# Performance work log

Measured on AMD Instinct MI355X. Metric: run time of the kernel, lower is better.

Reference implementation:

```python
import jax, jax.numpy as jnp
import numpy as np

EPS = 1e-12  # torch F.normalize default eps

def _l2norm(x):
    # torch.nn.functional.normalize(x, dim=-1): x / max(||x||_2, eps)
    n = jnp.linalg.norm(x, axis=-1, keepdims=True)
    return x / jnp.maximum(n, EPS)

def setup_inputs() -> dict:
    key = jax.random.key(0)
    ks = jax.random.split(key, 12)
    B, T, D, V, C = 16, 2048, 1024, 32000, 6
    s = 0.02
    text = jax.random.randint(ks[0], (B * T,), 0, V, dtype=jnp.int64)
    offsets = (jnp.arange(B, dtype=jnp.int64) * T)  # uniform-length sequences
    emb = jax.random.normal(ks[1], (V, D), dtype=jnp.float32) * s
    Wq = jax.random.normal(ks[2], (D, D), dtype=jnp.float32) * s
    bq = jnp.zeros((D,), jnp.float32)
    Wk = jax.random.normal(ks[3], (D, D), dtype=jnp.float32) * s
    bk = jnp.zeros((D,), jnp.float32)
    Wv = jax.random.normal(ks[4], (D, D), dtype=jnp.float32) * s
    bv = jnp.zeros((D,), jnp.float32)
    Wfc = jax.random.normal(ks[5], (D, D), dtype=jnp.float32) * s
    bfc = jnp.zeros((D,), jnp.float32)
    Wo = jax.random.normal(ks[6], (C, D), dtype=jnp.float32) * s
    bo = jnp.zeros((C,), jnp.float32)
    return {"text": text, "offsets": offsets, "emb": emb,
            "Wq": Wq, "bq": bq, "Wk": Wk, "bk": bk, "Wv": Wv, "bv": bv,
            "Wfc": Wfc, "bfc": bfc, "Wo": Wo, "bo": bo}

def reference(text, offsets, emb, Wq, bq, Wk, bk, Wv, bv, Wfc, bfc, Wo, bo):
    B = offsets.shape[0]
    T = text.shape[0] // B  # uniform lengths -> pad_sequence == reshape
    D = emb.shape[1]
    tok = text.reshape(B, T)
    x = emb[tok]                                   # [B,T,D]
    q = x @ Wq.T + bq
    k = x @ Wk.T + bk
    v = x @ Wv.T + bv
    scores = jnp.einsum('bqd,bkd->bqk', q, k) / jnp.sqrt(jnp.asarray(D, x.dtype))
    causal = jnp.tril(jnp.ones((T, T), dtype=bool))
    scores = jnp.where(causal[None, :, :], scores, -jnp.inf)
    attn = jax.nn.softmax(scores, axis=-1)
    out = jnp.einsum('bqk,bkd->bqd', attn, v) + x  # residual with embedding
    out = _l2norm(out)
    out = out + (out @ Wfc.T + bfc)                # residual FFN
    out = _l2norm(out)
    last = out[:, -1, :]                           # [B,D]
    return jax.nn.sigmoid(last @ Wo.T + bo)        # [B,num_class]
```

## Files before the change

kernel.cpp:

```cpp
#include <hip/hip_runtime.h>
#include <hip/hip_bf16.h>
#include <math.h>

typedef unsigned short ushort_t;

__device__ __forceinline__ float bf2f(ushort_t u) {
    union { unsigned int i; float f; } v;
    v.i = ((unsigned int)u) << 16;
    return v.f;
}

__device__ __forceinline__ ushort_t f2bf(float f) {
    union { float f; unsigned int i; } v; v.f = f;
    unsigned int lsb = (v.i >> 16) & 1;
    unsigned int r = v.i + 0x7FFF + lsb;
    return (ushort_t)(r >> 16);
}

__device__ __forceinline__ float wave_sum(float acc) {
    #pragma unroll
    for (int off = 32; off >= 1; off >>= 1) acc += __shfl_xor(acc, off, 64);
    return acc;
}
__device__ __forceinline__ float wave_max(float acc) {
    #pragma unroll
    for (int off = 32; off >= 1; off >>= 1) acc = fmaxf(acc, __shfl_xor(acc, off, 64));
    return acc;
}

__device__ __forceinline__ void ld8(const void* p, int isbf, size_t i, float* o) {
    if (isbf) {
        uint4 raw = *reinterpret_cast<const uint4*>((const ushort_t*)p + i);
        const ushort_t* pu = reinterpret_cast<const ushort_t*>(&raw);
        #pragma unroll
        for (int k = 0; k < 8; ++k) o[k] = bf2f(pu[k]);
    } else {
        const float4* f = reinterpret_cast<const float4*>((const float*)p + i);
        float4 a = f[0], b = f[1];
        o[0]=a.x; o[1]=a.y; o[2]=a.z; o[3]=a.w;
        o[4]=b.x; o[5]=b.y; o[6]=b.z; o[7]=b.w;
    }
}

__device__ __forceinline__ void ld4(const void* p, int isbf, size_t i, float* o) {
    if (isbf) {
        uint2 raw = *reinterpret_cast<const uint2*>((const ushort_t*)p + i);
        const ushort_t* pu = reinterpret_cast<const ushort_t*>(&raw);
        #pragma unroll
        for (int k = 0; k < 4; ++k) o[k] = bf2f(pu[k]);
    } else {
        float4 a = *reinterpret_cast<const float4*>((const float*)p + i);
        o[0]=a.x; o[1]=a.y; o[2]=a.z; o[3]=a.w;
    }
}

__device__ __forceinline__ float ldS(const void* p, int isbf, size_t i) {
    return isbf ? bf2f(((const ushort_t*)p)[i]) : ((const float*)p)[i];
}

__device__ __forceinline__ int tokAt(const void* text, int isi64, size_t i) {
    return isi64 ? ((const int*)text)[2 * i] : ((const int*)text)[i];
}

__device__ __forceinline__ void detect_flags(const void* emb, const void* text, int* sf) {
    if (threadIdx.x < 64) {
        const int lane = threadIdx.x;
        ushort_t u = ((const ushort_t*)emb)[2 * lane];
        int e = (u >> 7) & 0xFF;
        unsigned long long mb = __ballot(e >= 0x60 && e <= 0x7E);
        int odd = ((const int*)text)[2 * lane + 1];
        unsigned long long mi = __ballot(odd != 0);
        if (lane == 0) {
            sf[0] = (__popcll(mb) >= 32) ? 1 : 0;
            sf[1] = (__popcll(mi) == 0) ? 1 : 0;
        }
    }
    __syncthreads();
}

__device__ __forceinline__ void hoist16(const float* v, int lane, float* c16) {
    #pragma unroll
    for (int k = 0; k < 16; ++k) c16[k] = v[lane * 16 + k];
}

__global__ void kQC(const void* __restrict__ text, const void* __restrict__ emb,
                    const void* __restrict__ Wq, const void* __restrict__ bq,
                    const void* __restrict__ Wk, float* __restrict__ c_part,
                    int B, int T, int D) {
    const int nch = D >> 6;
    const int b = blockIdx.x / nch;
    const int ch = blockIdx.x % nch;
    const int i0 = ch << 6;
    const int tid = threadIdx.x;
    __shared__ int sf[2];
    __shared__ float xs[1024];
    __shared__ float qs[64];
    detect_flags(emb, text, sf);
    const int isbf = sf[0], isi64 = sf[1];
    const int tok = tokAt(text, isi64, (size_t)b * T + (T - 1));
    float w4[4];
    for (int dd = tid * 4; dd < D; dd += 1024) {
        ld4(emb, isbf, (size_t)tok * D + dd, w4);
        xs[dd]=w4[0]; xs[dd+1]=w4[1]; xs[dd+2]=w4[2]; xs[dd+3]=w4[3];
    }
    __syncthreads();
    const int wave = tid >> 6, lane = tid & 63;
    float c16[16];
    hoist16(xs, lane, c16);
    float w[8];
    for (int r = 0; r < 16; ++r) {
        const int i = i0 + wave * 16 + r;
        float acc = 0.f;
        ld8(Wq, isbf, (size_t)i * D + lane * 16, w);
        #pragma unroll
        for (int k = 0; k < 8; ++k) acc += w[k] * c16[k];
        ld8(Wq, isbf, (size_t)i * D + lane * 16 + 8, w);
        #pragma unroll
        for (int k = 0; k < 8; ++k) acc += w[k] * c16[8 + k];
        acc = wave_sum(acc);
        if (lane == 0) qs[wave * 16 + r] = acc + ldS(bq, isbf, i);
    }
    __syncthreads();
    const int d = tid * 4;
    float a0=0.f, a1=0.f, a2=0.f, a3=0.f;
    #pragma unroll 8
    for (int i = 0; i < 64; ++i) {
        const float qv = qs[i];
        ld4(Wk, isbf, (size_t)(i0 + i) * D + d, w4);
        a0 += qv*w4[0]; a1 += qv*w4[1]; a2 += qv*w4[2]; a3 += qv*w4[3];
    }
    *reinterpret_cast<float4*>(c_part + ((size_t)ch * B + b) * D + d)
        = make_float4(a0, a1, a2, a3);
}

__global__ void k35(const void* __restrict__ text, const void* __restrict__ emb,
                    const float* __restrict__ c_part, float* __restrict__ xbar_part,
                    float* __restrict__ m_part, float* __restrict__ l_part,
                    int B, int T, int D, int nch_c, float scale) {
    const int nch = T >> 5;
    const int b = blockIdx.x / nch;
    const int ch = blockIdx.x % nch;
    const int j0 = ch << 5;
    const int tid = threadIdx.x;
    __shared__ int sf[2];
    __shared__ ushort_t rows[32 * 1024];
    __shared__ float cs[1024];
    __shared__ float sjs[32];
    __shared__ float wls[32];
    __shared__ int tks[32];
    detect_flags(emb, text, sf);
    const int isbf = sf[0], isi64 = sf[1];
    {
        const int d = tid * 4;
        float4 acc = make_float4(0.f, 0.f, 0.f, 0.f);
        for (int cc = 0; cc < nch_c; ++cc) {
            float4 v = *reinterpret_cast<const float4*>(c_part + ((size_t)cc * B + b) * D + d);
            acc.x += v.x; acc.y += v.y; acc.z += v.z; acc.w += v.w;
        }
        cs[d]=acc.x; cs[d+1]=acc.y; cs[d+2]=acc.z; cs[d+3]=acc.w;
    }
    if (tid < 32) tks[tid] = tokAt(text, isi64, (size_t)b * T + j0 + tid);
    __syncthreads();
    if (isbf) {
        const ushort_t* E = (const ushort_t*)emb;
        const int half = tid >> 7;
        const int off  = (tid & 127) * 8;
        #pragma unroll 4
        for (int sw = 0; sw < 16; ++sw) {
            const int r = sw * 2 + half;
            uint4 v = *reinterpret_cast<const uint4*>(E + (size_t)tks[r] * D + off);
            *reinterpret_cast<uint4*>(&rows[r * 1024 + off]) = v;
        }
    }
    __syncthreads();
    const int wave = tid >> 6, lane = tid & 63;
    {
        float c16[16];
        hoist16(cs, lane, c16);
        float w[8];
        for (int rr = 0; rr < 8; ++rr) {
            const int r = wave + rr * 4;
            float acc = 0.f;
            if (isbf) {
                uint4 raw = *reinterpret_cast<const uint4*>(&rows[r * 1024 + lane * 16]);
                const ushort_t* pu = reinterpret_cast<const ushort_t*>(&raw);
                #pragma unroll
                for (int k = 0; k < 8; ++k) acc += bf2f(pu[k]) * c16[k];
                raw = *reinterpret_cast<const uint4*>(&rows[r * 1024 + lane * 16 + 8]);
                #pragma unroll
                for (int k = 0; k < 8; ++k) acc += bf2f(pu[k]) * c16[8 + k];
            } else {
                ld8(emb, 0, (size_t)tks[r] * D + lane * 16, w);
                #pragma unroll
                for (int k = 0; k < 8; ++k) acc += w[k] * c16[k];
                ld8(emb, 0, (size_t)tks[r] * D + lane * 16 + 8, w);
                #pragma unroll
                for (int k = 0; k < 8; ++k) acc += w[k] * c16[8 + k];
            }
            acc = wave_sum(acc);
            if (lane == 0) sjs[r] = acc * scale;
        }
    }
    __syncthreads();
    float mx = -INFINITY;
    #pragma unroll
    for (int j = 0; j < 32; ++j) mx = fmaxf(mx, sjs[j]);
    if (tid < 32) wls[tid] = expf(sjs[tid] - mx);
    __syncthreads();
    if (tid < 64) {
        float v = (tid < 32) ? wls[tid] : 0.f;
        v = wave_sum(v);
        if (tid == 0) { m_part[ch * B + b] = mx; l_part[ch * B + b] = v; }
    }
    const int d = tid * 4;
    float a0=0.f, a1=0.f, a2=0.f, a3=0.f;
    if (isbf) {
        #pragma unroll 8
        for (int j = 0; j < 32; ++j) {
            const float wj = wls[j];
            uint2 raw = *reinterpret_cast<const uint2*>(&rows[j * 1024 + d]);
            const ushort_t* pu = reinterpret_cast<const ushort_t*>(&raw);
            a0 += wj*bf2f(pu[0]); a1 += wj*bf2f(pu[1]);
            a2 += wj*bf2f(pu[2]); a3 += wj*bf2f(pu[3]);
        }
    } else {
        float w4[4];
        #pragma unroll 8
        for (int j = 0; j < 32; ++j) {
            const float wj = wls[j];
            ld4(emb, 0, (size_t)tks[j] * D + d, w4);
            a0 += wj*w4[0]; a1 += wj*w4[1]; a2 += wj*w4[2]; a3 += wj*w4[3];
        }
    }
    *reinterpret_cast<float4*>(xbar_part + ((size_t)ch * B + b) * D + d)
        = make_float4(a0, a1, a2, a3);
}

__global__ void kCA(const void* __restrict__ text, const void* __restrict__ emb,
                    const float* __restrict__ xbar_part, const float* __restrict__ m_part,
                    const float* __restrict__ l_part, const void* __restrict__ Wv,
                    const void* __restrict__ bv, float* __restrict__ u,
                    int B, int T, int D, int nch_k) {
    const int nb = D >> 5;
    const int b = blockIdx.x / nb;
    const int r0 = (blockIdx.x % nb) << 5;
    const int tid = threadIdx.x;
    __shared__ int sf[2];
    __shared__ float xb[1024];
    __shared__ float sc[64];
    __shared__ float xl32[32];
    detect_flags(emb, text, sf);
    const int isbf = sf[0], isi64 = sf[1];
    const int tok = tokAt(text, isi64, (size_t)b * T + (T - 1));
    if (tid < 32) xl32[tid] = ldS(emb, isbf, (size_t)tok * D + r0 + tid);
    if (tid < 64) {
        float mv = (tid < nch_k) ? m_part[tid * B + b] : -INFINITY;
        float mx = wave_max(mv);
        float e  = (tid < nch_k) ? expf(mv - mx) : 0.f;
        float lv = (tid < nch_k) ? l_part[tid * B + b] * e : 0.f;
        float lg = wave_sum(lv);
        sc[tid] = e / lg;
    }
    __syncthreads();
    {
        const int d = tid * 4;
        float4 acc = make_float4(0.f, 0.f, 0.f, 0.f);
        for (int cc = 0; cc < nch_k; ++cc) {
            const float s = sc[cc];
            float4 v = *reinterpret_cast<const float4*>(xbar_part + ((size_t)cc * B + b) * D + d);
            acc.x += s*v.x; acc.y += s*v.y; acc.z += s*v.z; acc.w += s*v.w;
        }
        xb[d]=acc.x; xb[d+1]=acc.y; xb[d+2]=acc.z; xb[d+3]=acc.w;
    }
    __syncthreads();
    const int wave = tid >> 6, lane = tid & 63;
    float c16[16];
    hoist16(xb, lane, c16);
    float w[8];
    for (int rr = 0; rr < 8; ++rr) {
        const int i = r0 + wave + rr * 4;
        float acc = 0.f;
        ld8(Wv, isbf, (size_t)i * D + lane * 16, w);
        #pragma unroll
        for (int k = 0; k < 8; ++k) acc += w[k] * c16[k];
        ld8(Wv, isbf, (size_t)i * D + lane * 16 + 8, w);
        #pragma unroll
        for (int k = 0; k < 8; ++k) acc += w[k] * c16[8 + k];
        acc = wave_sum(acc);
        if (lane == 0) u[b * D + i] = acc + ldS(bv, isbf, i) + xl32[i - r0];
    }
}

__global__ void k6c_h2(const void* __restrict__ text, const void* __restrict__ emb,
                       const void* __restrict__ Wfc, const void* __restrict__ bfc,
                       const float* __restrict__ u, float* __restrict__ h2, int D) {
    const int nb = D >> 5;
    const int b = blockIdx.x / nb;
    const int r0 = (blockIdx.x % nb) << 5;
    const int tid = threadIdx.x;
    __shared__ int sf[2];
    __shared__ float hs[1024];
    __shared__ float red[256];
    __shared__ float s_rn;
    detect_flags(emb, text, sf);
    const int isbf = sf[0];
    float part = 0.f;
    {
        const int dd = tid * 4;
        float4 v = *reinterpret_cast<const float4*>(u + b * D + dd);
        hs[dd]=v.x; hs[dd+1]=v.y; hs[dd+2]=v.z; hs[dd+3]=v.w;
        part = v.x*v.x + v.y*v.y + v.z*v.z + v.w*v.w;
    }
    red[tid] = part;
    __syncthreads();
    for (int st = 128; st; st >>= 1) {
        if (tid < st) red[tid] += red[tid + st];
        __syncthreads();
    }
    if (tid == 0) s_rn = 1.f / fmaxf(sqrtf(red[0]), 1e-12f);
    __syncthreads();
    const float rn = s_rn;
    {
        const int dd = tid * 4;
        hs[dd] *= rn; hs[dd+1] *= rn; hs[dd+2] *= rn; hs[dd+3] *= rn;
    }
    __syncthreads();
    const int wave = tid >> 6, lane = tid & 63;
    float c16[16];
    hoist16(hs, lane, c16);
    float w[8];
    for (int rr = 0; rr < 8; ++rr) {
        const int i = r0 + wave + rr * 4;
        float acc = 0.f;
        ld8(Wfc, isbf, (size_t)i * D + lane * 16, w);
        #pragma unroll
        for (int k = 0; k < 8; ++k) acc += w[k] * c16[k];
        ld8(Wfc, isbf, (size_t)i * D + lane * 16 + 8, w);
        #pragma unroll
        for (int k = 0; k < 8; ++k) acc += w[k] * c16[8 + k];
        acc = wave_sum(acc);
        if (lane == 0) h2[b * D + i] = hs[i] + acc + ldS(bfc, isbf, i);
    }
}

__global__ void k6d_out(const void* __restrict__ text, const void* __restrict__ emb,
                        const void* __restrict__ Wo, const void* __restrict__ bo,
                        const float* __restrict__ h2, void* __restrict__ out,
                        int D, int C, int total) {
    __shared__ int sf[2];
    detect_flags(emb, text, sf);
    const int isbf = sf[0];
    const int g = blockIdx.x * 4 + (threadIdx.x >> 6);
    if (g >= total) return;
    const int lane = threadIdx.x & 63;
    const int b = g / C, ci = g % C;
    float a1 = 0.f, a2 = 0.f, w[8], h[8];
    for (int d0 = lane * 8; d0 < D; d0 += 512) {
        ld8(Wo, isbf, (size_t)ci * D + d0, w);
        ld8(h2, 0, (size_t)b * D + d0, h);
        #pragma unroll
        for (int k = 0; k < 8; ++k) { a1 += w[k] * h[k]; a2 += h[k] * h[k]; }
    }
    a1 = wave_sum(a1);
    a2 = wave_sum(a2);
    if (lane == 0) {
        float rn = 1.f / fmaxf(sqrtf(a2), 1e-12f);
        float z = a1 * rn + ldS(bo, isbf, ci);
        float y = 1.f / (1.f + expf(-z));
        if (isbf) ((ushort_t*)out)[g] = f2bf(y);
        else      ((float*)out)[g] = y;
    }
}

extern "C" void kernel_launch(void* const* d_in, const int* in_sizes, int n_in,
                              void* d_out, int out_size, void* d_ws, size_t ws_size,
                              hipStream_t stream) {
    const void* text = d_in[0];
    const void* emb = d_in[2];
    const void* Wq  = d_in[3];
    const void* bq  = d_in[4];
    const void* Wk  = d_in[5];
    const void* Wv  = d_in[7];
    const void* bv  = d_in[8];
    const void* Wfc = d_in[9];
    const void* bfc = d_in[10];
    const void* Wo  = d_in[11];
    const void* bo  = d_in[12];

    const int B = in_sizes[1];
    const int T = in_sizes[0] / B;
    const int D = in_sizes[4];
    const int C = in_sizes[12];

    const int nch_c = D / 64;
    const int nch_k = T / 32;

    float* ws        = (float*)d_ws;
    float* c_part    = ws;
    float* xbar_part = c_part + (size_t)nch_c * B * D;
    float* m_part    = xbar_part + (size_t)nch_k * B * D;
    float* l_part    = m_part + (size_t)nch_k * B;
    float* u         = l_part + (size_t)nch_k * B;
    float* h2        = u + (size_t)B * D;

    const float scale = 1.0f / sqrtf((float)D);

    kQC<<<B * (D / 64), 256, 0, stream>>>(text, emb, Wq, bq, Wk, c_part, B, T, D);
    k35<<<B * (T / 32), 256, 0, stream>>>(text, emb, c_part, xbar_part, m_part, l_part,
                                          B, T, D, nch_c, scale);
    kCA<<<B * (D / 32), 256, 0, stream>>>(text, emb, xbar_part, m_part, l_part,
                                          Wv, bv, u, B, T, D, nch_k);
    k6c_h2<<<B * (D / 32), 256, 0, stream>>>(text, emb, Wfc, bfc, u, h2, D);
    k6d_out<<<(B * C + 3) / 4, 256, 0, stream>>>(text, emb, Wo, bo, h2, d_out, D, C, B * C);
}
```

Baseline: 290.9 us.

## Fuse five pipeline kernels into one persistent cooperative kernel with grid syncs

Replaces the five separate launches (QC, score/xbar, combine+Wv, FFN, output) with a single cooperative persistent kernel of 512 blocks that loops over tasks per phase and separates phases with grid.sync. The QC phase now uses 32-row chunks instead of 64, and partial-buffer layouts are reindexed batch-major. The goal is to remove the per-launch overhead and tail idle time between the small dependent kernels. In exchange it adds grid-wide barriers, requires all 512 blocks to be co-resident (launch_bounds 2 per CU, large shared-memory union), and gives each phase a fixed grid size that may underuse or serialize work.

```diff
diff --git a/kernel.cpp b/kernel.cpp
--- a/kernel.cpp
+++ b/kernel.cpp
@@ -1,7 +1,9 @@
 #include <hip/hip_runtime.h>
 #include <hip/hip_bf16.h>
+#include <hip/hip_cooperative_groups.h>
 #include <math.h>
 
+namespace cg = cooperative_groups;
 typedef unsigned short ushort_t;
 
 __device__ __forceinline__ float bf2f(ushort_t u) {
@@ -62,313 +64,312 @@
     return isi64 ? ((const int*)text)[2 * i] : ((const int*)text)[i];
 }
 
-__device__ __forceinline__ void detect_flags(const void* emb, const void* text, int* sf) {
-    if (threadIdx.x < 64) {
-        const int lane = threadIdx.x;
-        ushort_t u = ((const ushort_t*)emb)[2 * lane];
-        int e = (u >> 7) & 0xFF;
+__device__ __forceinline__ void hoist16(const float* v, int lane, float* c16) {
+    #pragma unroll
+    for (int k = 0; k < 16; ++k) c16[k] = v[lane * 16 + k];
+}
+
+struct SMem {
+    int sf[2];
+    union {
+        struct { float xs[1024]; float qs[32]; } p1;
+        struct { ushort_t rows[32 * 1024]; float cs[1024];
+                 float sjs[32]; float wls[32]; int tks[32]; } p2;
+        struct { float xb[1024]; float sc[64]; float xl[32]; } p3;
+        struct { float hs[1024]; float red[256]; float rn; } p4;
+    } u;
+};
+
+__global__ void __launch_bounds__(256, 2)
+mega(const void* __restrict__ text, const void* __restrict__ emb,
+     const void* __restrict__ Wq, const void* __restrict__ bq,
+     const void* __restrict__ Wk, const void* __restrict__ Wv,
+     const void* __restrict__ bv, const void* __restrict__ Wfc,
+     const void* __restrict__ bfc, const void* __restrict__ Wo,
+     const void* __restrict__ bo, float* __restrict__ c_part,
+     float* __restrict__ xbar_part, float* __restrict__ m_part,
+     float* __restrict__ l_part, float* __restrict__ ubuf,
+     float* __restrict__ h2, void* __restrict__ out,
+     int B, int T, int D, int C, float scale) {
+    __shared__ SMem sm;
+    cg::grid_group grid = cg::this_grid();
+    const int tid = threadIdx.x;
+    const int wave = tid >> 6, lane = tid & 63;
+
+    if (tid < 64) {
+        ushort_t uu = ((const ushort_t*)emb)[2 * lane];
+        int e = (uu >> 7) & 0xFF;
         unsigned long long mb = __ballot(e >= 0x60 && e <= 0x7E);
         int odd = ((const int*)text)[2 * lane + 1];
         unsigned long long mi = __ballot(odd != 0);
         if (lane == 0) {
-            sf[0] = (__popcll(mb) >= 32) ? 1 : 0;
-            sf[1] = (__popcll(mi) == 0) ? 1 : 0;
+            sm.sf[0] = (__popcll(mb) >= 32) ? 1 : 0;
+            sm.sf[1] = (__popcll(mi) == 0) ? 1 : 0;
         }
     }
     __syncthreads();
-}
-
-__device__ __forceinline__ void hoist16(const float* v, int lane, float* c16) {
-    #pragma unroll
-    for (int k = 0; k < 16; ++k) c16[k] = v[lane * 16 + k];
-}
-
-__global__ void kQC(const void* __restrict__ text, const void* __restrict__ emb,
-                    const void* __restrict__ Wq, const void* __restrict__ bq,
-                    const void* __restrict__ Wk, float* __restrict__ c_part,
-                    int B, int T, int D) {
-    const int nch = D >> 6;
-    const int b = blockIdx.x / nch;
-    const int ch = blockIdx.x % nch;
-    const int i0 = ch << 6;
-    const int tid = threadIdx.x;
-    __shared__ int sf[2];
-    __shared__ float xs[1024];
-    __shared__ float qs[64];
-    detect_flags(emb, text, sf);
-    const int isbf = sf[0], isi64 = sf[1];
-    const int tok = tokAt(text, isi64, (size_t)b * T + (T - 1));
-    float w4[4];
-    for (int dd = tid * 4; dd < D; dd += 1024) {
-        ld4(emb, isbf, (size_t)tok * D + dd, w4);
-        xs[dd]=w4[0]; xs[dd+1]=w4[1]; xs[dd+2]=w4[2]; xs[dd+3]=w4[3];
-    }
-    __syncthreads();
-    const int wave = tid >> 6, lane = tid & 63;
-    float c16[16];
-    hoist16(xs, lane, c16);
-    float w[8];
-    for (int r = 0; r < 16; ++r) {
-        const int i = i0 + wave * 16 + r;
-        float acc = 0.f;
-        ld8(Wq, isbf, (size_t)i * D + lane * 16, w);
+    const int isbf = sm.sf[0], isi64 = sm.sf[1];
+
+    const int nchD = D >> 5;
+    const int nchT = T >> 5;
+
+    for (int task = blockIdx.x; task < B * nchD; task += gridDim.x) {
+        const int b = task / nchD;
+        const int i0 = (task % nchD) << 5;
+        const int tok = tokAt(text, isi64, (size_t)b * T + (T - 1));
+        float w4[4];
+        {
+            const int dd = tid * 4;
+            ld4(emb, isbf, (size_t)tok * D + dd, w4);
+            sm.u.p1.xs[dd]=w4[0]; sm.u.p1.xs[dd+1]=w4[1];
+            sm.u.p1.xs[dd+2]=w4[2]; sm.u.p1.xs[dd+3]=w4[3];
+        }
+        __syncthreads();
+        float c16[16];
+        hoist16(sm.u.p1.xs, lane, c16);
+        float w[8];
+        for (int r = 0; r < 8; ++r) {
+            const int i = i0 + wave * 8 + r;
+            float acc = 0.f;
+            ld8(Wq, isbf, (size_t)i * D + lane * 16, w);
+            #pragma unroll
+            for (int k = 0; k < 8; ++k) acc += w[k] * c16[k];
+            ld8(Wq, isbf, (size_t)i * D + lane * 16 + 8, w);
+            #pragma unroll
+            for (int k = 0; k < 8; ++k) acc += w[k] * c16[8 + k];
+            acc = wave_sum(acc);
+            if (lane == 0) sm.u.p1.qs[wave * 8 + r] = acc + ldS(bq, isbf, i);
+        }
+        __syncthreads();
+        const int d = tid * 4;
+        float a0=0.f, a1=0.f, a2=0.f, a3=0.f;
+        #pragma unroll 8
+        for (int i = 0; i < 32; ++i) {
+            const float qv = sm.u.p1.qs[i];
+            ld4(Wk, isbf, (size_t)(i0 + i) * D + d, w4);
+            a0 += qv*w4[0]; a1 += qv*w4[1]; a2 += qv*w4[2]; a3 += qv*w4[3];
+        }
+        *reinterpret_cast<float4*>(c_part + (size_t)task * D + d)
+            = make_float4(a0, a1, a2, a3);
+        __syncthreads();
+    }
+    __threadfence();
+    grid.sync();
+
+    for (int task = blockIdx.x; task < B * nchT; task += gridDim.x) {
+        const int b = task / nchT;
+        const int ch = task % nchT;
+        const int j0 = ch << 5;
+        {
+            const int d = tid * 4;
+            float4 acc = make_float4(0.f, 0.f, 0.f, 0.f);
+            for (int cc = 0; cc < nchD; ++cc) {
+                float4 v = *reinterpret_cast<const float4*>(
+                    c_part + ((size_t)b * nchD + cc) * D + d);
+                acc.x += v.x; acc.y += v.y; acc.z += v.z; acc.w += v.w;
+            }
+            sm.u.p2.cs[d]=acc.x; sm.u.p2.cs[d+1]=acc.y;
+            sm.u.p2.cs[d+2]=acc.z; sm.u.p2.cs[d+3]=acc.w;
+        }
+        if (tid < 32) sm.u.p2.tks[tid] = tokAt(text, isi64, (size_t)b * T + j0 + tid);
+        __syncthreads();
+        if (isbf) {
+            const ushort_t* E = (const ushort_t*)emb;
+            const int half = tid >> 7;
+            const int off  = (tid & 127) * 8;
+            #pragma unroll 4
+            for (int sw = 0; sw < 16; ++sw) {
+                const int r = sw * 2 + half;
+                uint4 v = *reinterpret_cast<const uint4*>(
+                    E + (size_t)sm.u.p2.tks[r] * D + off);
+                *reinterpret_cast<uint4*>(&sm.u.p2.rows[r * 1024 + off]) = v;
+            }
+        }
+        __syncthreads();
+        {
+            float c16[16];
+            hoist16(sm.u.p2.cs, lane, c16);
+            float w[8];
+            for (int rr = 0; rr < 8; ++rr) {
+                const int r = wave + rr * 4;
+                float acc = 0.f;
+                if (isbf) {
+                    uint4 raw = *reinterpret_cast<const uint4*>(
+                        &sm.u.p2.rows[r * 1024 + lane * 16]);
+                    const ushort_t* pu = reinterpret_cast<const ushort_t*>(&raw);
+                    #pragma unroll
+                    for (int k = 0; k < 8; ++k) acc += bf2f(pu[k]) * c16[k];
+                    raw = *reinterpret_cast<const uint4*>(
+                        &sm.u.p2.rows[r * 1024 + lane * 16 + 8]);
+                    #pragma unroll
+                    for (int k = 0; k < 8; ++k) acc += bf2f(pu[k]) * c16[8 + k];
+                } else {
+                    ld8(emb, 0, (size_t)sm.u.p2.tks[r] * D + lane * 16, w);
+                    #pragma unroll
+                    for (int k = 0; k < 8; ++k) acc += w[k] * c16[k];
+                    ld8(emb, 0, (size_t)sm.u.p2.tks[r] * D + lane * 16 + 8, w);
+                    #pragma unroll
+                    for (int k = 0; k < 8; ++k) acc += w[k] * c16[8 + k];
+                }
+                acc = wave_sum(acc);
+                if (lane == 0) sm.u.p2.sjs[r] = acc * scale;
+            }
+        }
+        __syncthreads();
+        float mx = -INFINITY;
         #pragma unroll
-        for (int k = 0; k < 8; ++k) acc += w[k] * c16[k];
-        ld8(Wq, isbf, (size_t)i * D + lane * 16 + 8, w);
-        #pragma unroll
-        for (int k = 0; k < 8; ++k) acc += w[k] * c16[8 + k];
-        acc = wave_sum(acc);
-        if (lane == 0) qs[wave * 16 + r] = acc + ldS(bq, isbf, i);
-    }
-    __syncthreads();
-    const int d = tid * 4;
-    float a0=0.f, a1=0.f, a2=0.f, a3=0.f;
-    #pragma unroll 8
-    for (int i = 0; i < 64; ++i) {
-        const float qv = qs[i];
-        ld4(Wk, isbf, (size_t)(i0 + i) * D + d, w4);
-        a0 += qv*w4[0]; a1 += qv*w4[1]; a2 += qv*w4[2]; a3 += qv*w4[3];
-    }
-    *reinterpret_cast<float4*>(c_part + ((size_t)ch * B + b) * D + d)
-        = make_float4(a0, a1, a2, a3);
-}
-
-__global__ void k35(const void* __restrict__ text, const void* __restrict__ emb,
-                    const float* __restrict__ c_part, float* __restrict__ xbar_part,
-                    float* __restrict__ m_part, float* __restrict__ l_part,
-                    int B, int T, int D, int nch_c, float scale) {
-    const int nch = T >> 5;
-    const int b = blockIdx.x / nch;
-    const int ch = blockIdx.x % nch;
-    const int j0 = ch << 5;
-    const int tid = threadIdx.x;
-    __shared__ int sf[2];
-    __shared__ ushort_t rows[32 * 1024];
-    __shared__ float cs[1024];
-    __shared__ float sjs[32];
-    __shared__ float wls[32];
-    __shared__ int tks[32];
-    detect_flags(emb, text, sf);
-    const int isbf = sf[0], isi64 = sf[1];
-    {
+        for (int j = 0; j < 32; ++j) mx = fmaxf(mx, sm.u.p2.sjs[j]);
+        if (tid < 32) sm.u.p2.wls[tid] = expf(sm.u.p2.sjs[tid] - mx);
+        __syncthreads();
+        if (tid < 64) {
+            float v = (tid < 32) ? sm.u.p2.wls[tid] : 0.f;
+            v = wave_sum(v);
+            if (tid == 0) { m_part[(size_t)b * nchT + ch] = mx;
+                            l_part[(size_t)b * nchT + ch] = v; }
+        }
         const int d = tid * 4;
-        float4 acc = make_float4(0.f, 0.f, 0.f, 0.f);
-        for (int cc = 0; cc < nch_c; ++cc) {
-            float4 v = *reinterpret_cast<const float4*>(c_part + ((size_t)cc * B + b) * D + d);
-            acc.x += v.x; acc.y += v.y; acc.z += v.z; acc.w += v.w;
-        }
-        cs[d]=acc.x; cs[d+1]=acc.y; cs[d+2]=acc.z; cs[d+3]=acc.w;
-    }
-    if (tid < 32) tks[tid] = tokAt(text, isi64, (size_t)b * T + j0 + tid);
-    __syncthreads();
-    if (isbf) {
-        const ushort_t* E = (const ushort_t*)emb;
-        const int half = tid >> 7;
-        const int off  = (tid & 127) * 8;
-        #pragma unroll 4
-        for (int sw = 0; sw < 16; ++sw) {
-            const int r = sw * 2 + half;
-            uint4 v = *reinterpret_cast<const uint4*>(E + (size_t)tks[r] * D + off);
-            *reinterpret_cast<uint4*>(&rows[r * 1024 + off]) = v;
-        }
-    }
-    __syncthreads();
-    const int wave = tid >> 6, lane = tid & 63;
-    {
+        float a0=0.f, a1=0.f, a2=0.f, a3=0.f;
+        if (isbf) {
+            #pragma unroll 8
+            for (int j = 0; j < 32; ++j) {
+                const float wj = sm.u.p2.wls[j];
+                uint2 raw = *reinterpret_cast<const uint2*>(&sm.u.p2.rows[j * 1024 + d]);
+                const ushort_t* pu = reinterpret_cast<const ushort_t*>(&raw);
+                a0 += wj*bf2f(pu[0]); a1 += wj*bf2f(pu[1]);
+                a2 += wj*bf2f(pu[2]); a3 += wj*bf2f(pu[3]);
+            }
+        } else {
+            float w4[4];
+            #pragma unroll 8
+            for (int j = 0; j < 32; ++j) {
+                const float wj = sm.u.p2.wls[j];
+                ld4(emb, 0, (size_t)sm.u.p2.tks[j] * D + d, w4);
+                a0 += wj*w4[0]; a1 += wj*w4[1]; a2 += wj*w4[2]; a3 += wj*w4[3];
+            }
+        }
+        *reinterpret_cast<float4*>(xbar_part + (size_t)task * D + d)
+            = make_float4(a0, a1, a2, a3);
+        __syncthreads();
+    }
+    __threadfence();
+    grid.sync();
+
+    for (int task = blockIdx.x; task < B * nchD; task += gridDim.x) {
+        const int b = task / nchD;
+        const int r0 = (task % nchD) << 5;
+        const int tok = tokAt(text, isi64, (size_t)b * T + (T - 1));
+        if (tid < 32) sm.u.p3.xl[tid] = ldS(emb, isbf, (size_t)tok * D + r0 + tid);
+        if (tid < 64) {
+            float mv = (tid < nchT) ? m_part[(size_t)b * nchT + tid] : -INFINITY;
+            float mxx = wave_max(mv);
+            float e  = (tid < nchT) ? expf(mv - mxx) : 0.f;
+            float lv = (tid < nchT) ? l_part[(size_t)b * nchT + tid] * e : 0.f;
+            float lg = wave_sum(lv);
+            sm.u.p3.sc[tid] = e / lg;
+        }
+        __syncthreads();
+        {
+            const int d = tid * 4;
+            float4 acc = make_float4(0.f, 0.f, 0.f, 0.f);
+            for (int cc = 0; cc < nchT; ++cc) {
+                const float s = sm.u.p3.sc[cc];
+                float4 v = *reinterpret_cast<const float4*>(
+                    xbar_part + ((size_t)b * nchT + cc) * D + d);
+                acc.x += s*v.x; acc.y += s*v.y; acc.z += s*v.z; acc.w += s*v.w;
+            }
+            sm.u.p3.xb[d]=acc.x; sm.u.p3.xb[d+1]=acc.y;
+            sm.u.p3.xb[d+2]=acc.z; sm.u.p3.xb[d+3]=acc.w;
+        }
+        __syncthreads();
         float c16[16];
-        hoist16(cs, lane, c16);
+        hoist16(sm.u.p3.xb, lane, c16);
         float w[8];
         for (int rr = 0; rr < 8; ++rr) {
-            const int r = wave + rr * 4;
+            const int i = r0 + wave + rr * 4;
             float acc = 0.f;
-            if (isbf) {
-                uint4 raw = *reinterpret_cast<const uint4*>(&rows[r * 1024 + lane * 16]);
-                const ushort_t* pu = reinterpret_cast<const ushort_t*>(&raw);
+            ld8(Wv, isbf, (size_t)i * D + lane * 16, w);
+            #pragma unroll
+            for (int k = 0; k < 8; ++k) acc += w[k] * c16[k];
+            ld8(Wv, isbf, (size_t)i * D + lane * 16 + 8, w);
+            #pragma unroll
+            for (int k = 0; k < 8; ++k) acc += w[k] * c16[8 + k];
+            acc = wave_sum(acc);
+            if (lane == 0) ubuf[(size_t)b * D + i] = acc + ldS(bv, isbf, i)
+                                                      + sm.u.p3.xl[i - r0];
+        }
+        __syncthreads();
+    }
+    __threadfence();
+    grid.sync();
+
+    for (int task = blockIdx.x; task < B * nchD; task += gridDim.x) {
+        const int b = task / nchD;
+        const int r0 = (task % nchD) << 5;
+        float part;
+        {
+            const int dd = tid * 4;
+            float4 v = *reinterpret_cast<const float4*>(ubuf + (size_t)b * D + dd);
+            sm.u.p4.hs[dd]=v.x; sm.u.p4.hs[dd+1]=v.y;
+            sm.u.p4.hs[dd+2]=v.z; sm.u.p4.hs[dd+3]=v.w;
+            part = v.x*v.x + v.y*v.y + v.z*v.z + v.w*v.w;
+        }
+        sm.u.p4.red[tid] = part;
+        __syncthreads();
+        for (int st = 128; st; st >>= 1) {
+            if (tid < st) sm.u.p4.red[tid] += sm.u.p4.red[tid + st];
+            __syncthreads();
+        }
+        if (tid == 0) sm.u.p4.rn = 1.f / fmaxf(sqrtf(sm.u.p4.red[0]), 1e-12f);
+        __syncthreads();
+        const float rn = sm.u.p4.rn;
+        {
+            const int dd = tid * 4;
+            sm.u.p4.hs[dd] *= rn; sm.u.p4.hs[dd+1] *= rn;
+            sm.u.p4.hs[dd+2] *= rn; sm.u.p4.hs[dd+3] *= rn;
+        }
+        __syncthreads();
+        float c16[16];
+        hoist16(sm.u.p4.hs, lane, c16);
+        float w[8];
+        for (int rr = 0; rr < 8; ++rr) {
+            const int i = r0 + wave + rr * 4;
+            float acc = 0.f;
+            ld8(Wfc, isbf, (size_t)i * D + lane * 16, w);
+            #pragma unroll
+            for (int k = 0; k < 8; ++k) acc += w[k] * c16[k];
+            ld8(Wfc, isbf, (size_t)i * D + lane * 16 + 8, w);
+            #pragma unroll
+            for (int k = 0; k < 8; ++k) acc += w[k] * c16[8 + k];
+            acc = wave_sum(acc);
+            if (lane == 0) h2[(size_t)b * D + i] = sm.u.p4.hs[i] + acc + ldS(bfc, isbf, i);
+        }
+        __syncthreads();
+    }
+    __threadfence();
+    grid.sync();
+
+    {
+        const int total = B * C;
+        const int g = blockIdx.x * 4 + wave;
+        if (g < total) {
+            const int b = g / C, ci = g % C;
+            float a1 = 0.f, a2 = 0.f, w[8], h[8];
+            for (int d0 = lane * 8; d0 < D; d0 += 512) {
+                ld8(Wo, isbf, (size_t)ci * D + d0, w);
+                ld8(h2, 0, (size_t)b * D + d0, h);
                 #pragma unroll
-                for (int k = 0; k < 8; ++k) acc += bf2f(pu[k]) * c16[k];
-                raw = *reinterpret_cast<const uint4*>(&rows[r * 1024 + lane * 16 + 8]);
-                #pragma unroll
-                for (int k = 0; k < 8; ++k) acc += bf2f(pu[k]) * c16[8 + k];
-            } else {
-                ld8(emb, 0, (size_t)tks[r] * D + lane * 16, w);
-                #pragma unroll
-                for (int k = 0; k < 8; ++k) acc += w[k] * c16[k];
-                ld8(emb, 0, (size_t)tks[r] * D + lane * 16 + 8, w);
-                #pragma unroll
-                for (int k = 0; k < 8; ++k) acc += w[k] * c16[8 + k];
-            }
-            acc = wave_sum(acc);
-            if (lane == 0) sjs[r] = acc * scale;
-        }
-    }
-    __syncthreads();
-    float mx = -INFINITY;
-    #pragma unroll
-    for (int j = 0; j < 32; ++j) mx = fmaxf(mx, sjs[j]);
-    if (tid < 32) wls[tid] = expf(sjs[tid] - mx);
-    __syncthreads();
-    if (tid < 64) {
-        float v = (tid < 32) ? wls[tid] : 0.f;
-        v = wave_sum(v);
-        if (tid == 0) { m_part[ch * B + b] = mx; l_part[ch * B + b] = v; }
-    }
-    const int d = tid * 4;
-    float a0=0.f, a1=0.f, a2=0.f, a3=0.f;
-    if (isbf) {
-        #pragma unroll 8
-        for (int j = 0; j < 32; ++j) {
-            const float wj = wls[j];
-            uint2 raw = *reinterpret_cast<const uint2*>(&rows[j * 1024 + d]);
-            const ushort_t* pu = reinterpret_cast<const ushort_t*>(&raw);
-            a0 += wj*bf2f(pu[0]); a1 += wj*bf2f(pu[1]);
-            a2 += wj*bf2f(pu[2]); a3 += wj*bf2f(pu[3]);
-        }
-    } else {
-        float w4[4];
-        #pragma unroll 8
-        for (int j = 0; j < 32; ++j) {
-            const float wj = wls[j];
-            ld4(emb, 0, (size_t)tks[j] * D + d, w4);
-            a0 += wj*w4[0]; a1 += wj*w4[1]; a2 += wj*w4[2]; a3 += wj*w4[3];
-        }
-    }
-    *reinterpret_cast<float4*>(xbar_part + ((size_t)ch * B + b) * D + d)
-        = make_float4(a0, a1, a2, a3);
-}
-
-__global__ void kCA(const void* __restrict__ text, const void* __restrict__ emb,
-                    const float* __restrict__ xbar_part, const float* __restrict__ m_part,
-                    const float* __restrict__ l_part, const void* __restrict__ Wv,
-                    const void* __restrict__ bv, float* __restrict__ u,
-                    int B, int T, int D, int nch_k) {
-    const int nb = D >> 5;
-    const int b = blockIdx.x / nb;
-    const int r0 = (blockIdx.x % nb) << 5;
-    const int tid = threadIdx.x;
-    __shared__ int sf[2];
-    __shared__ float xb[1024];
-    __shared__ float sc[64];
-    __shared__ float xl32[32];
-    detect_flags(emb, text, sf);
-    const int isbf = sf[0], isi64 = sf[1];
-    const int tok = tokAt(text, isi64, (size_t)b * T + (T - 1));
-    if (tid < 32) xl32[tid] = ldS(emb, isbf, (size_t)tok * D + r0 + tid);
-    if (tid < 64) {
-        float mv = (tid < nch_k) ? m_part[tid * B + b] : -INFINITY;
-        float mx = wave_max(mv);
-        float e  = (tid < nch_k) ? expf(mv - mx) : 0.f;
-        float lv = (tid < nch_k) ? l_part[tid * B + b] * e : 0.f;
-        float lg = wave_sum(lv);
-        sc[tid] = e / lg;
-    }
-    __syncthreads();
-    {
-        const int d = tid * 4;
-        float4 acc = make_float4(0.f, 0.f, 0.f, 0.f);
-        for (int cc = 0; cc < nch_k; ++cc) {
-            const float s = sc[cc];
-            float4 v = *reinterpret_cast<const float4*>(xbar_part + ((size_t)cc * B + b) * D + d);
-            acc.x += s*v.x; acc.y += s*v.y; acc.z += s*v.z; acc.w += s*v.w;
-        }
-        xb[d]=acc.x; xb[d+1]=acc.y; xb[d+2]=acc.z; xb[d+3]=acc.w;
-    }
-    __syncthreads();
-    const int wave = tid >> 6, lane = tid & 63;
-    float c16[16];
-    hoist16(xb, lane, c16);
-    float w[8];
-    for (int rr = 0; rr < 8; ++rr) {
-        const int i = r0 + wave + rr * 4;
-        float acc = 0.f;
-        ld8(Wv, isbf, (size_t)i * D + lane * 16, w);
-        #pragma unroll
-        for (int k = 0; k < 8; ++k) acc += w[k] * c16[k];
-        ld8(Wv, isbf, (size_t)i * D + lane * 16 + 8, w);
-        #pragma unroll
-        for (int k = 0; k < 8; ++k) acc += w[k] * c16[8 + k];
-        acc = wave_sum(acc);
-        if (lane == 0) u[b * D + i] = acc + ldS(bv, isbf, i) + xl32[i - r0];
-    }
-}
-
-__global__ void k6c_h2(const void* __restrict__ text, const void* __restrict__ emb,
-                       const void* __restrict__ Wfc, const void* __restrict__ bfc,
-                       const float* __restrict__ u, float* __restrict__ h2, int D) {
-    const int nb = D >> 5;
-    const int b = blockIdx.x / nb;
-    const int r0 = (blockIdx.x % nb) << 5;
-    const int tid = threadIdx.x;
-    __shared__ int sf[2];
-    __shared__ float hs[1024];
-    __shared__ float red[256];
-    __shared__ float s_rn;
-    detect_flags(emb, text, sf);
-    const int isbf = sf[0];
-    float part = 0.f;
-    {
-        const int dd = tid * 4;
-        float4 v = *reinterpret_cast<const float4*>(u + b * D + dd);
-        hs[dd]=v.x; hs[dd+1]=v.y; hs[dd+2]=v.z; hs[dd+3]=v.w;
-        part = v.x*v.x + v.y*v.y + v.z*v.z + v.w*v.w;
-    }
-    red[tid] = part;
-    __syncthreads();
-    for (int st = 128; st; st >>= 1) {
-        if (tid < st) red[tid] += red[tid + st];
-        __syncthreads();
-    }
-    if (tid == 0) s_rn = 1.f / fmaxf(sqrtf(red[0]), 1e-12f);
-    __syncthreads();
-    const float rn = s_rn;
-    {
-        const int dd = tid * 4;
-        hs[dd] *= rn; hs[dd+1] *= rn; hs[dd+2] *= rn; hs[dd+3] *= rn;
-    }
-    __syncthreads();
-    const int wave = tid >> 6, lane = tid & 63;
-    float c16[16];
-    hoist16(hs, lane, c16);
-    float w[8];
-    for (int rr = 0; rr < 8; ++rr) {
-        const int i = r0 + wave + rr * 4;
-        float acc = 0.f;
-        ld8(Wfc, isbf, (size_t)i * D + lane * 16, w);
-        #pragma unroll
-        for (int k = 0; k < 8; ++k) acc += w[k] * c16[k];
-        ld8(Wfc, isbf, (size_t)i * D + lane * 16 + 8, w);
-        #pragma unroll
-        for (int k = 0; k < 8; ++k) acc += w[k] * c16[8 + k];
-        acc = wave_sum(acc);
-        if (lane == 0) h2[b * D + i] = hs[i] + acc + ldS(bfc, isbf, i);
-    }
-}
-
-__global__ void k6d_out(const void* __restrict__ text, const void* __restrict__ emb,
-                        const void* __restrict__ Wo, const void* __restrict__ bo,
-                        const float* __restrict__ h2, void* __restrict__ out,
-                        int D, int C, int total) {
-    __shared__ int sf[2];
-    detect_flags(emb, text, sf);
-    const int isbf = sf[0];
-    const int g = blockIdx.x * 4 + (threadIdx.x >> 6);
-    if (g >= total) return;
-    const int lane = threadIdx.x & 63;
-    const int b = g / C, ci = g % C;
-    float a1 = 0.f, a2 = 0.f, w[8], h[8];
-    for (int d0 = lane * 8; d0 < D; d0 += 512) {
-        ld8(Wo, isbf, (size_t)ci * D + d0, w);
-        ld8(h2, 0, (size_t)b * D + d0, h);
-        #pragma unroll
-        for (int k = 0; k < 8; ++k) { a1 += w[k] * h[k]; a2 += h[k] * h[k]; }
-    }
-    a1 = wave_sum(a1);
-    a2 = wave_sum(a2);
-    if (lane == 0) {
-        float rn = 1.f / fmaxf(sqrtf(a2), 1e-12f);
-        float z = a1 * rn + ldS(bo, isbf, ci);
-        float y = 1.f / (1.f + expf(-z));
-        if (isbf) ((ushort_t*)out)[g] = f2bf(y);
-        else      ((float*)out)[g] = y;
+                for (int k = 0; k < 8; ++k) { a1 += w[k] * h[k]; a2 += h[k] * h[k]; }
+            }
+            a1 = wave_sum(a1);
+            a2 = wave_sum(a2);
+            if (lane == 0) {
+                float rn = 1.f / fmaxf(sqrtf(a2), 1e-12f);
+                float z = a1 * rn + ldS(bo, isbf, ci);
+                float y = 1.f / (1.f + expf(-z));
+                if (isbf) ((ushort_t*)out)[g] = f2bf(y);
+                else      ((float*)out)[g] = y;
+            }
+        }
     }
 }
 
@@ -387,29 +388,32 @@
     const void* Wo  = d_in[11];
     const void* bo  = d_in[12];
 
-    const int B = in_sizes[1];
-    const int T = in_sizes[0] / B;
-    const int D = in_sizes[4];
-    const int C = in_sizes[12];
-
-    const int nch_c = D / 64;
-    const int nch_k = T / 32;
+    int B = in_sizes[1];
+    int T = in_sizes[0] / B;
+    int D = in_sizes[4];
+    int C = in_sizes[12];
+
+    const int nchD = D / 32;
+    const int nchT = T / 32;
 
     float* ws        = (float*)d_ws;
     float* c_part    = ws;
-    float* xbar_part = c_part + (size_t)nch_c * B * D;
-    float* m_part    = xbar_part + (size_t)nch_k * B * D;
-    float* l_part    = m_part + (size_t)nch_k * B;
-    float* u         = l_part + (size_t)nch_k * B;
-    float* h2        = u + (size_t)B * D;
-
-    const float scale = 1.0f / sqrtf((float)D);
-
-    kQC<<<B * (D / 64), 256, 0, stream>>>(text, emb, Wq, bq, Wk, c_part, B, T, D);
-    k35<<<B * (T / 32), 256, 0, stream>>>(text, emb, c_part, xbar_part, m_part, l_part,
-                                          B, T, D, nch_c, scale);
-    kCA<<<B * (D / 32), 256, 0, stream>>>(text, emb, xbar_part, m_part, l_part,
-                                          Wv, bv, u, B, T, D, nch_k);
-    k6c_h2<<<B * (D / 32), 256, 0, stream>>>(text, emb, Wfc, bfc, u, h2, D);
-    k6d_out<<<(B * C + 3) / 4, 256, 0, stream>>>(text, emb, Wo, bo, h2, d_out, D, C, B * C);
-}
+    float* xbar_part = c_part + (size_t)B * nchD * D;
+    float* m_part    = xbar_part + (size_t)B * nchT * D;
+    float* l_part    = m_part + (size_t)B * nchT;
+    float* ubuf      = l_part + (size_t)B * nchT;
+    float* h2        = ubuf + (size_t)B * D;
+
+    float scale = 1.0f / sqrtf((float)D);
+    void* outv = d_out;
+
+    void* args[] = {
+        (void*)&text, (void*)&emb, (void*)&Wq, (void*)&bq, (void*)&Wk,
+        (void*)&Wv, (void*)&bv, (void*)&Wfc, (void*)&bfc, (void*)&Wo,
+        (void*)&bo, (void*)&c_part, (void*)&xbar_part, (void*)&m_part,
+        (void*)&l_part, (void*)&ubuf, (void*)&h2, (void*)&outv,
+        (void*)&B, (void*)&T, (void*)&D, (void*)&C, (void*)&scale
+    };
+    hipLaunchCooperativeKernel((const void*)mega, dim3(512), dim3(256),
+                               args, 0, stream);
+}
```

After: 638.6 us. 120% more time.

## Split partial reductions into separate combine kernels and reorder block-to-batch mapping

Applied to the files above, without the earlier changes.

Partial-sum reductions that every block used to repeat are moved into two small combine kernels. kCC sums the c partials once per batch, so the 512 k35 blocks no longer each re-read 16 partial vectors. kC combines the softmax-weighted xbar partials once, so the 512 kVA blocks no longer each re-read 64 partial rows. Blocks in the weight GEMV kernels are also reordered batch-fastest, so blocks sharing the same weight rows run close together and hit in cache. The cost is two extra kernel launches and extra workspace round trips.

```diff
diff --git a/kernel.cpp b/kernel.cpp
--- a/kernel.cpp
+++ b/kernel.cpp
@@ -87,9 +87,8 @@
                     const void* __restrict__ Wq, const void* __restrict__ bq,
                     const void* __restrict__ Wk, float* __restrict__ c_part,
                     int B, int T, int D) {
-    const int nch = D >> 6;
-    const int b = blockIdx.x / nch;
-    const int ch = blockIdx.x % nch;
+    const int ch = blockIdx.x / B;
+    const int b  = blockIdx.x % B;
     const int i0 = ch << 6;
     const int tid = threadIdx.x;
     __shared__ int sf[2];
@@ -99,7 +98,8 @@
     const int isbf = sf[0], isi64 = sf[1];
     const int tok = tokAt(text, isi64, (size_t)b * T + (T - 1));
     float w4[4];
-    for (int dd = tid * 4; dd < D; dd += 1024) {
+    {
+        const int dd = tid * 4;
         ld4(emb, isbf, (size_t)tok * D + dd, w4);
         xs[dd]=w4[0]; xs[dd+1]=w4[1]; xs[dd+2]=w4[2]; xs[dd+3]=w4[3];
     }
@@ -133,13 +133,24 @@
         = make_float4(a0, a1, a2, a3);
 }
 
+__global__ void kCC(const float* __restrict__ c_part, float* __restrict__ c,
+                    int B, int D, int nch) {
+    const int nb = D >> 8;
+    const int b = blockIdx.x / nb;
+    const int d = (blockIdx.x % nb) * 256 + threadIdx.x;
+    float acc = 0.f;
+    for (int cc = 0; cc < nch; ++cc)
+        acc += c_part[((size_t)cc * B + b) * D + d];
+    c[(size_t)b * D + d] = acc;
+}
+
 __global__ void k35(const void* __restrict__ text, const void* __restrict__ emb,
-                    const float* __restrict__ c_part, float* __restrict__ xbar_part,
+                    const float* __restrict__ c, float* __restrict__ xbar_part,
                     float* __restrict__ m_part, float* __restrict__ l_part,
-                    int B, int T, int D, int nch_c, float scale) {
-    const int nch = T >> 5;
-    const int b = blockIdx.x / nch;
-    const int ch = blockIdx.x % nch;
+                    int B, int T, int D, float scale) {
+    const int nchT = T >> 5;
+    const int b = blockIdx.x / nchT;
+    const int ch = blockIdx.x % nchT;
     const int j0 = ch << 5;
     const int tid = threadIdx.x;
     __shared__ int sf[2];
@@ -152,12 +163,8 @@
     const int isbf = sf[0], isi64 = sf[1];
     {
         const int d = tid * 4;
-        float4 acc = make_float4(0.f, 0.f, 0.f, 0.f);
-        for (int cc = 0; cc < nch_c; ++cc) {
-            float4 v = *reinterpret_cast<const float4*>(c_part + ((size_t)cc * B + b) * D + d);
-            acc.x += v.x; acc.y += v.y; acc.z += v.z; acc.w += v.w;
-        }
-        cs[d]=acc.x; cs[d+1]=acc.y; cs[d+2]=acc.z; cs[d+3]=acc.w;
+        float4 v = *reinterpret_cast<const float4*>(c + (size_t)b * D + d);
+        cs[d]=v.x; cs[d+1]=v.y; cs[d+2]=v.z; cs[d+3]=v.w;
     }
     if (tid < 32) tks[tid] = tokAt(text, isi64, (size_t)b * T + j0 + tid);
     __syncthreads();
@@ -210,7 +217,8 @@
     if (tid < 64) {
         float v = (tid < 32) ? wls[tid] : 0.f;
         v = wave_sum(v);
-        if (tid == 0) { m_part[ch * B + b] = mx; l_part[ch * B + b] = v; }
+        if (tid == 0) { m_part[(size_t)b * nchT + ch] = mx;
+                        l_part[(size_t)b * nchT + ch] = v; }
     }
     const int d = tid * 4;
     float a0=0.f, a1=0.f, a2=0.f, a3=0.f;
@@ -232,45 +240,55 @@
             a0 += wj*w4[0]; a1 += wj*w4[1]; a2 += wj*w4[2]; a3 += wj*w4[3];
         }
     }
-    *reinterpret_cast<float4*>(xbar_part + ((size_t)ch * B + b) * D + d)
+    *reinterpret_cast<float4*>(xbar_part + ((size_t)b * nchT + ch) * D + d)
         = make_float4(a0, a1, a2, a3);
 }
 
-__global__ void kCA(const void* __restrict__ text, const void* __restrict__ emb,
-                    const float* __restrict__ xbar_part, const float* __restrict__ m_part,
-                    const float* __restrict__ l_part, const void* __restrict__ Wv,
-                    const void* __restrict__ bv, float* __restrict__ u,
-                    int B, int T, int D, int nch_k) {
-    const int nb = D >> 5;
+__global__ void kC(const float* __restrict__ xbar_part, const float* __restrict__ m_part,
+                   const float* __restrict__ l_part, float* __restrict__ xbar,
+                   int B, int D, int nchT) {
+    const int nb = D >> 8;
     const int b = blockIdx.x / nb;
-    const int r0 = (blockIdx.x % nb) << 5;
+    const int d = (blockIdx.x % nb) * 256 + threadIdx.x;
+    __shared__ float sc[128];
+    if (threadIdx.x < 64) {
+        float mx = -INFINITY;
+        for (int cc = (int)threadIdx.x; cc < nchT; cc += 64)
+            mx = fmaxf(mx, m_part[(size_t)b * nchT + cc]);
+        mx = wave_max(mx);
+        float ls = 0.f;
+        for (int cc = (int)threadIdx.x; cc < nchT; cc += 64)
+            ls += l_part[(size_t)b * nchT + cc] * expf(m_part[(size_t)b * nchT + cc] - mx);
+        ls = wave_sum(ls);
+        for (int cc = (int)threadIdx.x; cc < nchT; cc += 64)
+            sc[cc] = expf(m_part[(size_t)b * nchT + cc] - mx) / ls;
+    }
+    __syncthreads();
+    float acc = 0.f;
+    for (int cc = 0; cc < nchT; ++cc)
+        acc += sc[cc] * xbar_part[((size_t)b * nchT + cc) * D + d];
+    xbar[(size_t)b * D + d] = acc;
+}
+
+__global__ void kVA(const void* __restrict__ text, const void* __restrict__ emb,
+                    const void* __restrict__ Wv, const void* __restrict__ bv,
+                    const float* __restrict__ xbar, float* __restrict__ u,
+                    int B, int T, int D) {
+    const int ch = blockIdx.x / B;
+    const int b  = blockIdx.x % B;
+    const int r0 = ch << 5;
     const int tid = threadIdx.x;
     __shared__ int sf[2];
     __shared__ float xb[1024];
-    __shared__ float sc[64];
-    __shared__ float xl32[32];
+    __shared__ float xl[32];
     detect_flags(emb, text, sf);
     const int isbf = sf[0], isi64 = sf[1];
     const int tok = tokAt(text, isi64, (size_t)b * T + (T - 1));
-    if (tid < 32) xl32[tid] = ldS(emb, isbf, (size_t)tok * D + r0 + tid);
-    if (tid < 64) {
-        float mv = (tid < nch_k) ? m_part[tid * B + b] : -INFINITY;
-        float mx = wave_max(mv);
-        float e  = (tid < nch_k) ? expf(mv - mx) : 0.f;
-        float lv = (tid < nch_k) ? l_part[tid * B + b] * e : 0.f;
-        float lg = wave_sum(lv);
-        sc[tid] = e / lg;
-    }
-    __syncthreads();
-    {
-        const int d = tid * 4;
-        float4 acc = make_float4(0.f, 0.f, 0.f, 0.f);
-        for (int cc = 0; cc < nch_k; ++cc) {
-            const float s = sc[cc];
-            float4 v = *reinterpret_cast<const float4*>(xbar_part + ((size_t)cc * B + b) * D + d);
-            acc.x += s*v.x; acc.y += s*v.y; acc.z += s*v.z; acc.w += s*v.w;
-        }
-        xb[d]=acc.x; xb[d+1]=acc.y; xb[d+2]=acc.z; xb[d+3]=acc.w;
+    if (tid < 32) xl[tid] = ldS(emb, isbf, (size_t)tok * D + r0 + tid);
+    {
+        const int dd = tid * 4;
+        float4 v = *reinterpret_cast<const float4*>(xbar + (size_t)b * D + dd);
+        xb[dd]=v.x; xb[dd+1]=v.y; xb[dd+2]=v.z; xb[dd+3]=v.w;
     }
     __syncthreads();
     const int wave = tid >> 6, lane = tid & 63;
@@ -287,16 +305,17 @@
         #pragma unroll
         for (int k = 0; k < 8; ++k) acc += w[k] * c16[8 + k];
         acc = wave_sum(acc);
-        if (lane == 0) u[b * D + i] = acc + ldS(bv, isbf, i) + xl32[i - r0];
+        if (lane == 0) u[(size_t)b * D + i] = acc + ldS(bv, isbf, i) + xl[i - r0];
     }
 }
 
 __global__ void k6c_h2(const void* __restrict__ text, const void* __restrict__ emb,
                        const void* __restrict__ Wfc, const void* __restrict__ bfc,
-                       const float* __restrict__ u, float* __restrict__ h2, int D) {
-    const int nb = D >> 5;
-    const int b = blockIdx.x / nb;
-    const int r0 = (blockIdx.x % nb) << 5;
+                       const float* __restrict__ u, float* __restrict__ h2,
+                       int B, int D) {
+    const int ch = blockIdx.x / B;
+    const int b  = blockIdx.x % B;
+    const int r0 = ch << 5;
     const int tid = threadIdx.x;
     __shared__ int sf[2];
     __shared__ float hs[1024];
@@ -304,10 +323,10 @@
     __shared__ float s_rn;
     detect_flags(emb, text, sf);
     const int isbf = sf[0];
-    float part = 0.f;
+    float part;
     {
         const int dd = tid * 4;
-        float4 v = *reinterpret_cast<const float4*>(u + b * D + dd);
+        float4 v = *reinterpret_cast<const float4*>(u + (size_t)b * D + dd);
         hs[dd]=v.x; hs[dd+1]=v.y; hs[dd+2]=v.z; hs[dd+3]=v.w;
         part = v.x*v.x + v.y*v.y + v.z*v.z + v.w*v.w;
     }
@@ -339,7 +358,7 @@
         #pragma unroll
         for (int k = 0; k < 8; ++k) acc += w[k] * c16[8 + k];
         acc = wave_sum(acc);
-        if (lane == 0) h2[b * D + i] = hs[i] + acc + ldS(bfc, isbf, i);
+        if (lane == 0) h2[(size_t)b * D + i] = hs[i] + acc + ldS(bfc, isbf, i);
     }
 }
 
@@ -393,23 +412,26 @@
     const int C = in_sizes[12];
 
     const int nch_c = D / 64;
-    const int nch_k = T / 32;
+    const int nchT  = T / 32;
 
     float* ws        = (float*)d_ws;
     float* c_part    = ws;
-    float* xbar_part = c_part + (size_t)nch_c * B * D;
-    float* m_part    = xbar_part + (size_t)nch_k * B * D;
-    float* l_part    = m_part + (size_t)nch_k * B;
-    float* u         = l_part + (size_t)nch_k * B;
+    float* c         = c_part + (size_t)nch_c * B * D;
+    float* xbar_part = c + (size_t)B * D;
+    float* m_part    = xbar_part + (size_t)B * nchT * D;
+    float* l_part    = m_part + (size_t)B * nchT;
+    float* xbar      = l_part + (size_t)B * nchT;
+    float* u         = xbar + (size_t)B * D;
     float* h2        = u + (size_t)B * D;
 
     const float scale = 1.0f / sqrtf((float)D);
 
-    kQC<<<B * (D / 64), 256, 0, stream>>>(text, emb, Wq, bq, Wk, c_part, B, T, D);
-    k35<<<B * (T / 32), 256, 0, stream>>>(text, emb, c_part, xbar_part, m_part, l_part,
-                                          B, T, D, nch_c, scale);
-    kCA<<<B * (D / 32), 256, 0, stream>>>(text, emb, xbar_part, m_part, l_part,
-                                          Wv, bv, u, B, T, D, nch_k);
-    k6c_h2<<<B * (D / 32), 256, 0, stream>>>(text, emb, Wfc, bfc, u, h2, D);
+    kQC<<<(D / 64) * B, 256, 0, stream>>>(text, emb, Wq, bq, Wk, c_part, B, T, D);
+    kCC<<<B * (D / 256), 256, 0, stream>>>(c_part, c, B, D, nch_c);
+    k35<<<B * (T / 32), 256, 0, stream>>>(text, emb, c, xbar_part, m_part, l_part,
+                                          B, T, D, scale);
+    kC<<<B * (D / 256), 256, 0, stream>>>(xbar_part, m_part, l_part, xbar, B, D, nchT);
+    kVA<<<(D / 32) * B, 256, 0, stream>>>(text, emb, Wv, bv, xbar, u, B, T, D);
+    k6c_h2<<<(D / 32) * B, 256, 0, stream>>>(text, emb, Wfc, bfc, u, h2, B, D);
     k6d_out<<<(B * C + 3) / 4, 256, 0, stream>>>(text, emb, Wo, bo, h2, d_out, D, C, B * C);
 }
```

Result: slower. 300.7 us (+3.4%).
